# Kernel optimization log

Measured on AMD Instinct MI355X. Metric: run time of the kernel, lower is better.

## Reference

```python
import jax, jax.numpy as jnp
import numpy as np

B, S, H, P2 = 64, 512, 768, 46  # batch, seq, hidden, num_p*2


def setup_inputs() -> dict:
    key = jax.random.key(0)
    k1, k2, k3, k4 = jax.random.split(key, 4)
    hidden_states = jax.random.normal(k1, (B, S, H), dtype=jnp.float32)
    # subject start/end indices must lie within the valid (masked-in) prefix
    lengths = jax.random.randint(k2, (B,), S // 4, S + 1)  # cue lengths per sample
    input_mask = (jnp.arange(S)[None, :] < lengths[:, None]).astype(jnp.int32)
    ids = jax.random.randint(k3, (B, 2), 0, S // 4)
    batch_subject_ids = jnp.sort(ids, axis=1).astype(jnp.int32)
    W = jax.random.normal(k4, (P2, H), dtype=jnp.float32) * (1.0 / np.sqrt(H))
    b = jnp.zeros((P2,), dtype=jnp.float32)
    return {"hidden_states": hidden_states, "batch_subject_ids": batch_subject_ids,
            "input_mask": input_mask, "W": W, "b": b}


def reference(hidden_states, batch_subject_ids, input_mask, W, b):
    # per-sample subject embedding: h[b, start] + h[b, end]  -> [B, H]
    batch_idx = jnp.arange(hidden_states.shape[0])
    s = (hidden_states[batch_idx, batch_subject_ids[:, 0]]
         + hidden_states[batch_idx, batch_subject_ids[:, 1]])
    # broadcast-add s to the first cue_len positions of each sample
    cue_len = jnp.sum(input_mask, axis=1)  # [B]
    pos_mask = (jnp.arange(hidden_states.shape[1])[None, :] < cue_len[:, None])  # [B, S]
    h = hidden_states + s[:, None, :] * pos_mask[:, :, None].astype(hidden_states.dtype)
    # linear + sigmoid^4 (dropout is identity in eval mode)
    logits = jnp.einsum('bsh,ph->bsp', h, W) + b
    return jax.nn.sigmoid(logits) ** 4
```

## Files before the change

### kernel.cpp

```cpp
#include <hip/hip_runtime.h>
#include <hip/hip_bf16.h>

#define SEQ 512
#define HID 768
#define P2  46
#define MT  64
#define BLK 256
#define NSTEP (HID / 32)
#define QSTRIDE 48

typedef short bf16x8 __attribute__((ext_vector_type(8)));
typedef float f32x4  __attribute__((ext_vector_type(4)));

__device__ __forceinline__ unsigned short f2bf(float f) {
  union { float f; unsigned int u; } v; v.f = f;
  return (unsigned short)((v.u + 0x7FFFu + ((v.u >> 16) & 1u)) >> 16);
}

__device__ __forceinline__ short fcvt(float f) {
  __hip_bfloat16 x = __float2bfloat16(f);
  return *reinterpret_cast<short*>(&x);
}

__global__ __launch_bounds__(64) void prep_kernel(
    const float* __restrict__ h, const int* __restrict__ ids,
    const float* __restrict__ W, unsigned short* __restrict__ Wb,
    float* __restrict__ q) {
  int b = blockIdx.x, p = blockIdx.y, lane = threadIdx.x;
  const float* w = W + (size_t)p * HID;
  if (b == 0) {
    #pragma unroll
    for (int j = 0; j < HID / 64; ++j)
      Wb[p * HID + lane + j * 64] = f2bf(w[lane + j * 64]);
  }
  int i0 = ids[b * 2 + 0], i1 = ids[b * 2 + 1];
  const float* r0 = h + ((size_t)b * SEQ + i0) * HID;
  const float* r1 = h + ((size_t)b * SEQ + i1) * HID;
  float acc = 0.f;
  #pragma unroll
  for (int j = 0; j < HID / 64; ++j) {
    int k = lane + j * 64;
    acc += (r0[k] + r1[k]) * w[k];
  }
  #pragma unroll
  for (int off = 32; off > 0; off >>= 1) acc += __shfl_down(acc, off, 64);
  if (lane == 0) q[b * QSTRIDE + p] = acc;
}

__global__ __launch_bounds__(BLK, 2) void main_kernel(
    const float* __restrict__ h, const int* __restrict__ mask,
    const unsigned short* __restrict__ Wb, const float* __restrict__ bias,
    const float* __restrict__ q, float* __restrict__ out) {
  const int tid  = threadIdx.x;
  const int lane = tid & 63, wv = tid >> 6;
  const int mr = lane & 15, qd = lane >> 4;
  const int row0 = blockIdx.x * MT;
  const int b    = row0 >> 9;
  const int row  = row0 + (wv << 4) + mr;

  const float* hb = h + (size_t)row * HID + (qd << 3);
  const unsigned short* wb = Wb + mr * HID + (qd << 3);

  float4 ph[8][2];
  #pragma unroll
  for (int s = 0; s < 8; ++s) {
    ph[s][0] = *(const float4*)(hb + (s << 5));
    ph[s][1] = *(const float4*)(hb + (s << 5) + 4);
  }
  bf16x8 pw[2][3];
  #pragma unroll
  for (int s = 0; s < 2; ++s)
    #pragma unroll
    for (int nt = 0; nt < 3; ++nt)
      pw[s][nt] = *(const bf16x8*)(wb + nt * 16 * HID + (s << 5));

  f32x4 acc[3];
  #pragma unroll
  for (int nt = 0; nt < 3; ++nt) acc[nt] = f32x4{0.f, 0.f, 0.f, 0.f};

  #pragma unroll
  for (int s = 0; s < NSTEP; ++s) {
    float4 c0 = ph[s & 7][0], c1 = ph[s & 7][1];
    if (s + 8 < NSTEP) {
      ph[s & 7][0] = *(const float4*)(hb + ((s + 8) << 5));
      ph[s & 7][1] = *(const float4*)(hb + ((s + 8) << 5) + 4);
    }
    bf16x8 hfrag = { fcvt(c0.x), fcvt(c0.y), fcvt(c0.z), fcvt(c0.w),
                     fcvt(c1.x), fcvt(c1.y), fcvt(c1.z), fcvt(c1.w) };
    bf16x8 w0 = pw[s & 1][0], w1 = pw[s & 1][1], w2 = pw[s & 1][2];
    if (s + 2 < NSTEP) {
      #pragma unroll
      for (int nt = 0; nt < 3; ++nt)
        pw[s & 1][nt] = *(const bf16x8*)(wb + nt * 16 * HID + ((s + 2) << 5));
    }
    acc[0] = __builtin_amdgcn_mfma_f32_16x16x32_bf16(w0, hfrag, acc[0], 0, 0, 0);
    acc[1] = __builtin_amdgcn_mfma_f32_16x16x32_bf16(w1, hfrag, acc[1], 0, 0, 0);
    acc[2] = __builtin_amdgcn_mfma_f32_16x16x32_bf16(w2, hfrag, acc[2], 0, 0, 0);
  }

  const int mk = mask[row];
  float* orow = out + (size_t)row * P2;
  const float* qrow = q + b * QSTRIDE;
  #pragma unroll
  for (int nt = 0; nt < 3; ++nt) {
    const int p0 = (nt << 4) + (qd << 2);
    float o[4];
    #pragma unroll
    for (int i = 0; i < 4; ++i) {
      float bv = (p0 + i < P2) ? bias[p0 + i] : 0.f;
      float qv = qrow[p0 + i];
      float x = acc[nt][i] + bv + (mk ? qv : 0.f);
      float sg = 1.f / (1.f + __expf(-x));
      sg *= sg; sg *= sg;
      o[i] = sg;
    }
    if (p0 + 1 < P2) *(float2*)(orow + p0)     = make_float2(o[0], o[1]);
    if (p0 + 3 < P2) *(float2*)(orow + p0 + 2) = make_float2(o[2], o[3]);
  }
}

extern "C" void kernel_launch(void* const* d_in, const int* in_sizes, int n_in,
                              void* d_out, int out_size, void* d_ws, size_t ws_size,
                              hipStream_t stream) {
  const float* h    = (const float*)d_in[0];
  const int*   ids  = (const int*)d_in[1];
  const int*   mask = (const int*)d_in[2];
  const float* W    = (const float*)d_in[3];
  const float* bias = (const float*)d_in[4];
  float* out = (float*)d_out;

  unsigned short* Wb = (unsigned short*)d_ws;
  float* q = (float*)((char*)d_ws + 48 * HID * sizeof(unsigned short));

  prep_kernel<<<dim3(64, P2), 64, 0, stream>>>(h, ids, W, Wb, q);
  main_kernel<<<dim3((64 * SEQ) / MT), BLK, 0, stream>>>(h, mask, Wb, bias, q, out);
}
```

Before: 166.1 us.

## Stage hidden tile in swizzled LDS as bf16 and split N-tiles across waves

The main kernel now loads a 32-row tile of hidden states cooperatively with 512 threads, converts it to bf16, and stores it in shared memory with an XOR swizzle to avoid bank conflicts. Six of the eight waves each compute one 16x16 output tile, one M-half by one N-tile, reading A fragments from LDS and W fragments from global memory. This replaces per-wave register prefetch pipelines with a block-wide staged load, and the prep kernel now zero-fills the two padded W rows. In exchange it adds a barrier, idles two waves during compute, and uses 48KB of LDS per block, which may limit occupancy.

After: 166.1 us. About the same (+0.0%).

```diff
diff --git a/kernel.cpp b/kernel.cpp
--- a/kernel.cpp
+++ b/kernel.cpp
@@ -4,8 +4,8 @@
 #define SEQ 512
 #define HID 768
 #define P2  46
-#define MT  64
-#define BLK 256
+#define MT  32
+#define BLK 512
 #define NSTEP (HID / 32)
 #define QSTRIDE 48
 
@@ -17,9 +17,9 @@
   return (unsigned short)((v.u + 0x7FFFu + ((v.u >> 16) & 1u)) >> 16);
 }
 
-__device__ __forceinline__ short fcvt(float f) {
+__device__ __forceinline__ unsigned short fcvt(float f) {
   __hip_bfloat16 x = __float2bfloat16(f);
-  return *reinterpret_cast<short*>(&x);
+  return *reinterpret_cast<unsigned short*>(&x);
 }
 
 __global__ __launch_bounds__(64) void prep_kernel(
@@ -32,6 +32,11 @@
     #pragma unroll
     for (int j = 0; j < HID / 64; ++j)
       Wb[p * HID + lane + j * 64] = f2bf(w[lane + j * 64]);
+    if (p < 2) {
+      #pragma unroll
+      for (int j = 0; j < HID / 64; ++j)
+        Wb[(P2 + p) * HID + lane + j * 64] = 0;
+    }
   }
   int i0 = ids[b * 2 + 0], i1 = ids[b * 2 + 1];
   const float* r0 = h + ((size_t)b * SEQ + i0) * HID;
@@ -47,76 +52,71 @@
   if (lane == 0) q[b * QSTRIDE + p] = acc;
 }
 
-__global__ __launch_bounds__(BLK, 2) void main_kernel(
+__global__ __launch_bounds__(BLK, 4) void main_kernel(
     const float* __restrict__ h, const int* __restrict__ mask,
     const unsigned short* __restrict__ Wb, const float* __restrict__ bias,
     const float* __restrict__ q, float* __restrict__ out) {
+  __shared__ __align__(16) unsigned short hA[MT][HID];
+
   const int tid  = threadIdx.x;
   const int lane = tid & 63, wv = tid >> 6;
   const int mr = lane & 15, qd = lane >> 4;
   const int row0 = blockIdx.x * MT;
   const int b    = row0 >> 9;
-  const int row  = row0 + (wv << 4) + mr;
 
-  const float* hb = h + (size_t)row * HID + (qd << 3);
-  const unsigned short* wb = Wb + mr * HID + (qd << 3);
+  const float* hblk = h + (size_t)row0 * HID;
+  #pragma unroll
+  for (int i = 0; i < 12; ++i) {
+    int g = i * BLK + tid;
+    float4 v = *(const float4*)(hblk + ((size_t)g << 2));
+    int r  = g / 192;
+    int f  = g - r * 192;
+    int c  = f >> 1, hc = f & 1;
+    int cs = (c & 0x78) | ((c ^ r) & 7);
+    ushort4 u;
+    u.x = fcvt(v.x); u.y = fcvt(v.y); u.z = fcvt(v.z); u.w = fcvt(v.w);
+    *(ushort4*)&hA[r][(cs << 3) + (hc << 2)] = u;
+  }
+  __syncthreads();
 
-  float4 ph[8][2];
+  if (wv >= 6) return;
+  const int wm = wv & 1, nt = wv >> 1;
+
+  const int rloc = (wm << 4) + mr;
+  const unsigned short* wbp = Wb + (size_t)((nt << 4) + mr) * HID + (qd << 3);
+
+  const int grow = row0 + rloc;
+  const int mk   = mask[grow];
+  const int p0   = (nt << 4) + (qd << 2);
+  const float* qrow = q + b * QSTRIDE;
+  float bv[4], qv[4];
   #pragma unroll
-  for (int s = 0; s < 8; ++s) {
-    ph[s][0] = *(const float4*)(hb + (s << 5));
-    ph[s][1] = *(const float4*)(hb + (s << 5) + 4);
+  for (int i = 0; i < 4; ++i) {
+    bv[i] = (p0 + i < P2) ? bias[p0 + i] : 0.f;
+    qv[i] = qrow[p0 + i];
   }
-  bf16x8 pw[2][3];
-  #pragma unroll
-  for (int s = 0; s < 2; ++s)
-    #pragma unroll
-    for (int nt = 0; nt < 3; ++nt)
-      pw[s][nt] = *(const bf16x8*)(wb + nt * 16 * HID + (s << 5));
 
-  f32x4 acc[3];
-  #pragma unroll
-  for (int nt = 0; nt < 3; ++nt) acc[nt] = f32x4{0.f, 0.f, 0.f, 0.f};
-
+  f32x4 acc = f32x4{0.f, 0.f, 0.f, 0.f};
   #pragma unroll
   for (int s = 0; s < NSTEP; ++s) {
-    float4 c0 = ph[s & 7][0], c1 = ph[s & 7][1];
-    if (s + 8 < NSTEP) {
-      ph[s & 7][0] = *(const float4*)(hb + ((s + 8) << 5));
-      ph[s & 7][1] = *(const float4*)(hb + ((s + 8) << 5) + 4);
-    }
-    bf16x8 hfrag = { fcvt(c0.x), fcvt(c0.y), fcvt(c0.z), fcvt(c0.w),
-                     fcvt(c1.x), fcvt(c1.y), fcvt(c1.z), fcvt(c1.w) };
-    bf16x8 w0 = pw[s & 1][0], w1 = pw[s & 1][1], w2 = pw[s & 1][2];
-    if (s + 2 < NSTEP) {
-      #pragma unroll
-      for (int nt = 0; nt < 3; ++nt)
-        pw[s & 1][nt] = *(const bf16x8*)(wb + nt * 16 * HID + ((s + 2) << 5));
-    }
-    acc[0] = __builtin_amdgcn_mfma_f32_16x16x32_bf16(w0, hfrag, acc[0], 0, 0, 0);
-    acc[1] = __builtin_amdgcn_mfma_f32_16x16x32_bf16(w1, hfrag, acc[1], 0, 0, 0);
-    acc[2] = __builtin_amdgcn_mfma_f32_16x16x32_bf16(w2, hfrag, acc[2], 0, 0, 0);
+    int c  = (s << 2) + qd;
+    int cs = (c & 0x78) | ((c ^ (rloc & 7)) & 7);
+    bf16x8 a  = *(const bf16x8*)&hA[rloc][cs << 3];
+    bf16x8 wf = *(const bf16x8*)(wbp + (s << 5));
+    acc = __builtin_amdgcn_mfma_f32_16x16x32_bf16(wf, a, acc, 0, 0, 0);
   }
 
-  const int mk = mask[row];
-  float* orow = out + (size_t)row * P2;
-  const float* qrow = q + b * QSTRIDE;
+  float* orow = out + (size_t)grow * P2;
+  float o[4];
   #pragma unroll
-  for (int nt = 0; nt < 3; ++nt) {
-    const int p0 = (nt << 4) + (qd << 2);
-    float o[4];
-    #pragma unroll
-    for (int i = 0; i < 4; ++i) {
-      float bv = (p0 + i < P2) ? bias[p0 + i] : 0.f;
-      float qv = qrow[p0 + i];
-      float x = acc[nt][i] + bv + (mk ? qv : 0.f);
-      float sg = 1.f / (1.f + __expf(-x));
-      sg *= sg; sg *= sg;
-      o[i] = sg;
-    }
-    if (p0 + 1 < P2) *(float2*)(orow + p0)     = make_float2(o[0], o[1]);
-    if (p0 + 3 < P2) *(float2*)(orow + p0 + 2) = make_float2(o[2], o[3]);
+  for (int i = 0; i < 4; ++i) {
+    float x = acc[i] + bv[i] + (mk ? qv[i] : 0.f);
+    float sg = 1.f / (1.f + __expf(-x));
+    sg *= sg; sg *= sg;
+    o[i] = sg;
   }
+  if (p0 + 1 < P2) *(float2*)(orow + p0)     = make_float2(o[0], o[1]);
+  if (p0 + 3 < P2) *(float2*)(orow + p0 + 2) = make_float2(o[2], o[3]);
 }
 
 extern "C" void kernel_launch(void* const* d_in, const int* in_sizes, int n_in,
```
